# Performance work log

Hardware: AMD Instinct MI355X
Metric: run time of the kernel (lower is better)

## Reference

```python
import jax, jax.numpy as jnp
import numpy as np

B, N, M, T = 120, 128, 192, 25
PHI_MIN, PHI_MAX = 1e-6, 30.0


def _phi(x):
    # phi(x) = -log(tanh(x/2)); self-inverse map used for exact sum-product CN update
    return -jnp.log(jnp.tanh(0.5 * jnp.clip(x, PHI_MIN, PHI_MAX)))


def setup_inputs() -> dict:
    rng = np.random.default_rng(0)
    Hx = (rng.random((M, N)) < 4.0 / N).astype(np.float32)   # weight-4 stabilizer-like rows
    Hz = (rng.random((M, N)) < 4.0 / N).astype(np.float32)
    Gx = (rng.random((2, N)) < 16.0 / N).astype(np.float32)  # logical checks for the loss
    Gz = (rng.random((2, N)) < 16.0 / N).astype(np.float32)
    errorx = (rng.random((B, N)) < 0.05).astype(np.float32)  # X-component indicator
    errorz = (rng.random((B, N)) < 0.05).astype(np.float32)  # Z-component indicator
    return {
        "errorx": jnp.asarray(errorx),
        "errorz": jnp.asarray(errorz),
        "ep0": jnp.full((1,), 0.1, jnp.float32),
        "Hx": jnp.asarray(Hx),
        "Hz": jnp.asarray(Hz),
        "Gx": jnp.asarray(Gx),
        "Gz": jnp.asarray(Gz),
        "weights_llr": jnp.ones((T,), jnp.float32),
        "weights_vn": jnp.ones((T,), jnp.float32),
        "weights_cn": jnp.ones((T,), jnp.float32),
    }


def reference(errorx, errorz, ep0, Hx, Hz, Gx, Gz, weights_llr, weights_vn, weights_cn):
    ep = ep0[0]
    # depolarizing channel LLR: P(X-component) = 2*ep/3
    llr0 = jnp.log((1.0 - 2.0 * ep / 3.0) / (2.0 * ep / 3.0))
    Hs = jnp.stack([Hz, Hx])                                   # (2,M,N): ch0 detects X errors, ch1 Z
    synx = jnp.remainder(errorx @ Hz.T, 2.0)                   # (B,M)
    synz = jnp.remainder(errorz @ Hx.T, 2.0)
    syn_sign = 1.0 - 2.0 * jnp.stack([synx, synz], axis=1)     # (B,2,M)
    HALF_PI = jnp.float32(np.pi / 2)

    def iter_loss(Gamma):
        # loss of eq. 11: soft corrections must reproduce a zero syndrome on G
        prob = jax.nn.sigmoid(-Gamma)
        pX, pZ = prob[:, 0, :], prob[:, 1, :]
        corrz = jnp.where(errorz > 0.5, 1.0 - pX, pX)          # qz/qy -> 1-pX, qx/qi -> pX
        corrx = jnp.where(errorx > 0.5, 1.0 - pZ, pZ)
        sx = jnp.einsum('gn,bn->bg', Gz, corrx)
        sz = jnp.einsum('gn,bn->bg', Gx, corrz)
        return (jnp.sum(jnp.abs(jnp.sin(HALF_PI * sz)), axis=1)
                + jnp.sum(jnp.abs(jnp.sin(HALF_PI * sx)), axis=1))

    def body(V, w):
        w_llr, w_vn, w_cn = w
        # --- check node update (exact box-plus via sign/phi decomposition) ---
        sgn = jnp.where(Hs > 0, jnp.where(V < 0, -1.0, 1.0), 1.0)
        tot_sgn = jnp.prod(sgn, axis=3, keepdims=True)         # (B,2,M,1)
        p = jnp.where(Hs > 0, _phi(jnp.abs(V)), 0.0)
        p_sum = jnp.sum(p, axis=3, keepdims=True)
        cn = syn_sign[..., None] * tot_sgn * sgn * _phi(p_sum - p) * Hs * w_cn
        # --- variable node update ---
        cn_sum = jnp.sum(cn, axis=2)                           # (B,2,N)
        Gamma = w_llr * llr0 + cn_sum                          # (B,2,N) marginal LLRs
        Vnew = (w_llr * llr0 + w_vn * (cn_sum[:, :, None, :] - cn)) * Hs
        return Vnew, iter_loss(Gamma)

    V0 = jnp.broadcast_to(llr0 * Hs, (errorx.shape[0], 2, Hs.shape[1], Hs.shape[2]))
    _, losses = jax.lax.scan(body, V0, (weights_llr, weights_vn, weights_cn))  # (T,B)
    loss = jnp.mean(jnp.sum(losses, axis=0))
    loss_min = jnp.mean(jnp.min(losses, axis=0))
    return jnp.stack([loss, loss_min])
```

## Files before the change

### kernel.cpp

```cpp
#include <hip/hip_runtime.h>
#include <math.h>

#define Bsz 120
#define Nv  128
#define Ms  192
#define Tit 25
#define EPAD 1024
#define KE4 4
#define DC  16
#define DV  24

#define O_VCOL 0
#define O_ECHK 512
#define O_VEID 1024
#define O_RP   2560
#define O_DEG  2656
#define SSTRIDE 2752
#define WS_CNT  (2 * SSTRIDE)
#define WS_PART (WS_CNT + 2)

__device__ __forceinline__ float phi_f(float x) {
  x = fminf(fmaxf(x, 1e-6f), 30.0f);
  const float u = __expf(-x);
  float den = 1.0f - u;
  if (x < 0.03125f) den = x * (1.0f - 0.5f * x + 0.16666667f * x * x);
  return 0.69314718f * (__log2f(1.0f + u) - __log2f(den));
}

#define USH(arr, k) ((arr[(k) >> 1] >> (((k) & 1) * 16)) & 0xffff)

__global__ __launch_bounds__(384) void setup_kernel(const float* __restrict__ Hx,
                                                    const float* __restrict__ Hz,
                                                    int* __restrict__ W) {
  __shared__ unsigned mask[2 * Ms][4];
  __shared__ int rp_s[2][Ms + 1];
  __shared__ int wtot[6];
  const int tid = threadIdx.x;
  const int lane = tid & 63, wv = tid >> 6;
  const int s = (tid >= Ms) ? 1 : 0;
  const int m = s ? tid - Ms : tid;
  const float* H = s ? Hx : Hz;
  unsigned short* vcol_g = (unsigned short*)(W + s * SSTRIDE + O_VCOL);
  unsigned short* echk_g = (unsigned short*)(W + s * SSTRIDE + O_ECHK);
  unsigned short* rp_g   = (unsigned short*)(W + s * SSTRIDE + O_RP);
  unsigned short* deg_g  = (unsigned short*)(W + s * SSTRIDE + O_DEG);

  if (tid == 0) W[WS_CNT] = 0;

  unsigned mw[4];
  int d = 0;
  const float4* H4 = (const float4*)(H + m * Nv);
#pragma unroll
  for (int w = 0; w < 4; ++w) {
    unsigned bits = 0;
#pragma unroll
    for (int q = 0; q < 8; ++q) {
      const float4 v = H4[w * 8 + q];
      if (v.x > 0.f) bits |= 1u << (q * 4 + 0);
      if (v.y > 0.f) bits |= 1u << (q * 4 + 1);
      if (v.z > 0.f) bits |= 1u << (q * 4 + 2);
      if (v.w > 0.f) bits |= 1u << (q * 4 + 3);
    }
    mw[w] = bits;
    mask[tid][w] = bits;
    d += __popc(bits);
  }
  int x = d;
#pragma unroll
  for (int off = 1; off < 64; off <<= 1) {
    const int y = __shfl_up(x, off);
    if (lane >= off) x += y;
  }
  if (lane == 63) wtot[wv] = x;
  __syncthreads();
  int carry = 0;
  const int wbase = s ? 3 : 0;
  for (int k = wbase; k < wv; ++k) carry += wtot[k];
  const int incl = x + carry;
  const int excl = incl - d;
  rp_s[s][m] = excl;
  if (m == Ms - 1) rp_s[s][Ms] = incl;
  rp_g[m] = (unsigned short)excl;
  deg_g[m] = (unsigned short)((d <= DC) ? d : DC);
  __syncthreads();
  const int E = rp_s[s][Ms];
  {
    int o = excl;
#pragma unroll
    for (int w = 0; w < 4; ++w) {
      unsigned bits = mw[w];
      while (bits) {
        const int j = __ffs(bits) - 1;
        bits &= bits - 1;
        if (o < EPAD) { vcol_g[o] = (unsigned short)(w * 32 + j); echk_g[o] = (unsigned short)m; }
        ++o;
      }
    }
  }
  for (int e = E + m; e < EPAD; e += Ms) { vcol_g[e] = Nv; echk_g[e] = Ms; }
  __syncthreads();
  if (tid < 2 * Nv) {
    const int s2 = tid >> 7, n = tid & (Nv - 1);
    const int wnd = n >> 5, bit = n & 31;
    unsigned short* veid_g = (unsigned short*)(W + s2 * SSTRIDE + O_VEID);
    int kk = 0;
    for (int m2 = 0; m2 < Ms; ++m2) {
      const unsigned wb = mask[s2 * Ms + m2][wnd];
      if ((wb >> bit) & 1u) {
        int ke = __popc(wb & ((1u << bit) - 1u));
        for (int w = 0; w < wnd; ++w) ke += __popc(mask[s2 * Ms + m2][w]);
        if (kk < DV) veid_g[n * DV + kk] = (unsigned short)(rp_s[s2][m2] + ke);
        ++kk;
      }
    }
    for (int z = (kk < DV ? kk : DV); z < DV; ++z) veid_g[n * DV + z] = EPAD;
  }
}

__global__ __launch_bounds__(256, 1) void nbp_kernel(
    const float* __restrict__ errorx, const float* __restrict__ errorz,
    const float* __restrict__ ep0,
    const float* __restrict__ Gx, const float* __restrict__ Gz,
    const float* __restrict__ w_llr, const float* __restrict__ w_vn,
    const float* __restrict__ w_cn,
    int* __restrict__ W, float* __restrict__ out) {
  __shared__ float p_l[EPAD + 1];
  __shared__ float cn_l[EPAD + 1];
  __shared__ float csum_l[Nv + 1];
  __shared__ float2 pt2[256];
  __shared__ float corrbuf[2][Nv];
  __shared__ float wls[Tit], wvs[Tit], wcs[Tit];
  __shared__ float wred[4], wredm[4];
  __shared__ int lastFlag;

  const int tid = threadIdx.x;
  const int bid = blockIdx.x;
  const int b = bid >> 1, s = bid & 1;
  const int* base = W + s * SSTRIDE;
  const unsigned short* vcol_g = (const unsigned short*)(base + O_VCOL);
  const unsigned short* echk_g = (const unsigned short*)(base + O_ECHK);
  const unsigned short* veid_g = (const unsigned short*)(base + O_VEID);
  const unsigned short* rp_g   = (const unsigned short*)(base + O_RP);
  const unsigned short* deg_g  = (const unsigned short*)(base + O_DEG);
  float* partBase = (float*)(W + WS_PART);
  float* part = partBase + (s * Bsz + b) * Tit;

  const float ep   = ep0[0];
  const float a23  = (2.0f * ep) / 3.0f;
  const float llr0 = logf((1.0f - a23) / a23);

  if (tid < Tit) {
    wls[tid] = w_llr[tid];
    wvs[tid] = w_vn[tid];
    wcs[tid] = w_cn[tid];
  }
  if (tid < Nv) {
    const float* esyn = (s ? errorz : errorx) + b * Nv;
    csum_l[tid] = esyn[tid];
  }
  if (tid == 0) {
    csum_l[Nv] = 0.f;
    p_l[EPAD] = 0.f;
    cn_l[EPAD] = 0.f;
  }

  unsigned vcolp[2] = {0, 0}, chkp[2] = {0, 0};
#pragma unroll
  for (int k = 0; k < KE4; ++k) {
    const unsigned vc = vcol_g[tid + (k << 8)];
    const unsigned ck = echk_g[tid + (k << 8)];
    vcolp[k >> 1] |= vc << ((k & 1) * 16);
    chkp[k >> 1]  |= ck << ((k & 1) * 16);
  }
  const int rp0 = (tid < Ms) ? (int)rp_g[tid] : 0;
  const int dg0 = (tid < Ms) ? (int)deg_g[tid] : 0;

  unsigned vep[12];
  float ec = 0.f;
  if (tid < Nv) {
    const uint4* q = (const uint4*)(veid_g + tid * DV);
    const uint4 a0 = q[0], a1 = q[1], a2 = q[2];
    vep[0] = a0.x; vep[1] = a0.y; vep[2]  = a0.z; vep[3]  = a0.w;
    vep[4] = a1.x; vep[5] = a1.y; vep[6]  = a1.z; vep[7]  = a1.w;
    vep[8] = a2.x; vep[9] = a2.y; vep[10] = a2.z; vep[11] = a2.w;
    ec = ((s ? errorx : errorz) + b * Nv)[tid];
  }
  const int l2 = tid - 128;
  float g0a = 0.f, g0b = 0.f, g1a = 0.f, g1b = 0.f;
  if (tid >= 128 && tid < 192) {
    const float* G = s ? Gz : Gx;
    g0a = G[l2]; g0b = G[l2 + 64];
    g1a = G[Nv + l2]; g1b = G[Nv + l2 + 64];
  }
  __syncthreads();

#pragma unroll
  for (int k = 0; k < KE4; ++k) {
    const int e = tid + (k << 8);
    const int nn = USH(vcolp, k);
    p_l[e] = (csum_l[nn] > 0.5f) ? -1.f : 1.f;
  }
  __syncthreads();
  float ssgn;
  {
    unsigned par = 0;
#pragma unroll
    for (int k = 0; k < DC; ++k) {
      const int addr = (k < dg0) ? (rp0 + k) : EPAD;
      par ^= __float_as_uint(p_l[addr]) >> 31;
    }
    ssgn = (par & 1u) ? -1.f : 1.f;
  }
  __syncthreads();

  float cn_reg[KE4] = {0.f, 0.f, 0.f, 0.f};
  float basePrev = llr0, wvPrev = 0.f;

#pragma unroll 1
  for (int t = 0; t < Tit; ++t) {
    const float wct = wcs[t];

    float pe[KE4];
#pragma unroll
    for (int k = 0; k < KE4; ++k) {
      const int e = tid + (k << 8);
      const int nn = USH(vcolp, k);
      const float csv = csum_l[nn];
      const float Vk = basePrev + wvPrev * (csv - cn_reg[k]);
      float pv = phi_f(fabsf(Vk));
      pv = fmaxf(pv, 1e-30f);
      pv = (Vk < 0.f) ? -pv : pv;
      pe[k] = pv;
      p_l[e] = pv;
    }
    __syncthreads();

    {
      float psum = 0.f;
      unsigned par = 0;
#pragma unroll
      for (int k = 0; k < DC; ++k) {
        const int addr = (k < dg0) ? (rp0 + k) : EPAD;
        const float v = p_l[addr];
        par ^= __float_as_uint(v) >> 31;
        psum += fabsf(v);
      }
      const float tt = ((par & 1u) ? -ssgn : ssgn) * wct;
      pt2[tid] = make_float2(psum, tt);
    }
    __syncthreads();

#pragma unroll
    for (int k = 0; k < KE4; ++k) {
      const int cc = USH(chkp, k);
      const float2 q = pt2[cc];
      const float ps = pe[k];
      const float sg = (__float_as_uint(ps) >> 31) ? -1.f : 1.f;
      const float cnk = q.y * sg * phi_f(q.x - fabsf(ps));
      cn_reg[k] = cnk;
      cn_l[tid + (k << 8)] = cnk;
    }
    __syncthreads();

    const float base_t = wls[t] * llr0;
    if (tid < Nv) {
      float cs = 0.f;
#pragma unroll
      for (int k = 0; k < DV; ++k) cs += cn_l[USH(vep, k)];
      csum_l[tid] = cs;
      const float prob = 1.0f / (1.0f + __expf(base_t + cs));
      corrbuf[t & 1][tid] = (ec > 0.5f) ? 1.0f - prob : prob;
    } else if (tid < 192 && t > 0) {
      const float* cr = corrbuf[(t - 1) & 1];
      const float c0 = cr[l2], c1 = cr[l2 + 64];
      float la = g0a * c0 + g0b * c1;
      float lb = g1a * c0 + g1b * c1;
#pragma unroll
      for (int off = 1; off < 64; off <<= 1) {
        la += __shfl_xor(la, off);
        lb += __shfl_xor(lb, off);
      }
      const float lt = fabsf(__sinf(1.57079632679f * la)) +
                       fabsf(__sinf(1.57079632679f * lb));
      if (l2 == 0) part[t - 1] = lt;
    }
    basePrev = base_t;
    wvPrev = wvs[t];
    __syncthreads();
  }

  if (tid >= 128 && tid < 192) {
    const float* cr = corrbuf[(Tit - 1) & 1];
    const float c0 = cr[l2], c1 = cr[l2 + 64];
    float la = g0a * c0 + g0b * c1;
    float lb = g1a * c0 + g1b * c1;
#pragma unroll
    for (int off = 1; off < 64; off <<= 1) {
      la += __shfl_xor(la, off);
      lb += __shfl_xor(lb, off);
    }
    const float lt = fabsf(__sinf(1.57079632679f * la)) +
                     fabsf(__sinf(1.57079632679f * lb));
    if (l2 == 0) part[Tit - 1] = lt;
  }
  __syncthreads();

  __threadfence();
  if (tid == 0) lastFlag = (atomicAdd(W + WS_CNT, 1) == 2 * Bsz - 1);
  __syncthreads();
  if (lastFlag) {
    __threadfence();
    float sm = 0.f, mn = 0.f;
    if (tid < Bsz) {
      const float* pa = partBase + tid * Tit;
      const float* pb = partBase + (Bsz + tid) * Tit;
      float acc = 0.f, mloc = 3.0e38f;
#pragma unroll
      for (int t = 0; t < Tit; ++t) {
        const float lt = pa[t] + pb[t];
        acc += lt;
        mloc = fminf(mloc, lt);
      }
      sm = acc;
      mn = mloc;
    }
#pragma unroll
    for (int off = 32; off; off >>= 1) {
      sm += __shfl_down(sm, off);
      mn += __shfl_down(mn, off);
    }
    if ((tid & 63) == 0) { wred[tid >> 6] = sm; wredm[tid >> 6] = mn; }
    __syncthreads();
    if (tid == 0) {
      out[0] = (wred[0] + wred[1]) * (1.0f / Bsz);
      out[1] = (wredm[0] + wredm[1]) * (1.0f / Bsz);
    }
  }
}

extern "C" void kernel_launch(void* const* d_in, const int* in_sizes, int n_in,
                              void* d_out, int out_size, void* d_ws, size_t ws_size,
                              hipStream_t stream) {
  const float* errorx = (const float*)d_in[0];
  const float* errorz = (const float*)d_in[1];
  const float* ep0    = (const float*)d_in[2];
  const float* Hx     = (const float*)d_in[3];
  const float* Hz     = (const float*)d_in[4];
  const float* Gx     = (const float*)d_in[5];
  const float* Gz     = (const float*)d_in[6];
  const float* wllr   = (const float*)d_in[7];
  const float* wvn    = (const float*)d_in[8];
  const float* wcn    = (const float*)d_in[9];
  float* out = (float*)d_out;
  int* W = (int*)d_ws;

  hipLaunchKernelGGL(setup_kernel, dim3(1), dim3(2 * Ms), 0, stream, Hx, Hz, W);
  hipLaunchKernelGGL(nbp_kernel, dim3(2 * Bsz), dim3(256), 0, stream,
                     errorx, errorz, ep0, Gx, Gz, wllr, wvn, wcn, W, out);
}
```

Before: 167.1 us.

## Fuse sparse-graph setup into the decoder kernel, building adjacency in shared memory

Removes the single-block setup kernel. Each decoder block now rebuilds the check-node and variable-node adjacency from Hx/Hz in shared memory, using a column bitmask built with shared atomics. A memset replaces the counter reset. This removes one serial kernel launch and the global round trip for the index tables, at the cost of every one of the 240 blocks repeating the setup work and using more shared memory.

```diff
diff --git a/kernel.cpp b/kernel.cpp
--- a/kernel.cpp
+++ b/kernel.cpp
@@ -10,14 +10,8 @@
 #define DC  16
 #define DV  24
 
-#define O_VCOL 0
-#define O_ECHK 512
-#define O_VEID 1024
-#define O_RP   2560
-#define O_DEG  2656
-#define SSTRIDE 2752
-#define WS_CNT  (2 * SSTRIDE)
-#define WS_PART (WS_CNT + 2)
+#define WS_CNT  0
+#define WS_PART 2
 
 __device__ __forceinline__ float phi_f(float x) {
   x = fminf(fmaxf(x, 1e-6f), 30.0f);
@@ -29,119 +23,34 @@
 
 #define USH(arr, k) ((arr[(k) >> 1] >> (((k) & 1) * 16)) & 0xffff)
 
-__global__ __launch_bounds__(384) void setup_kernel(const float* __restrict__ Hx,
-                                                    const float* __restrict__ Hz,
-                                                    int* __restrict__ W) {
-  __shared__ unsigned mask[2 * Ms][4];
-  __shared__ int rp_s[2][Ms + 1];
-  __shared__ int wtot[6];
-  const int tid = threadIdx.x;
-  const int lane = tid & 63, wv = tid >> 6;
-  const int s = (tid >= Ms) ? 1 : 0;
-  const int m = s ? tid - Ms : tid;
-  const float* H = s ? Hx : Hz;
-  unsigned short* vcol_g = (unsigned short*)(W + s * SSTRIDE + O_VCOL);
-  unsigned short* echk_g = (unsigned short*)(W + s * SSTRIDE + O_ECHK);
-  unsigned short* rp_g   = (unsigned short*)(W + s * SSTRIDE + O_RP);
-  unsigned short* deg_g  = (unsigned short*)(W + s * SSTRIDE + O_DEG);
-
-  if (tid == 0) W[WS_CNT] = 0;
-
-  unsigned mw[4];
-  int d = 0;
-  const float4* H4 = (const float4*)(H + m * Nv);
-#pragma unroll
-  for (int w = 0; w < 4; ++w) {
-    unsigned bits = 0;
-#pragma unroll
-    for (int q = 0; q < 8; ++q) {
-      const float4 v = H4[w * 8 + q];
-      if (v.x > 0.f) bits |= 1u << (q * 4 + 0);
-      if (v.y > 0.f) bits |= 1u << (q * 4 + 1);
-      if (v.z > 0.f) bits |= 1u << (q * 4 + 2);
-      if (v.w > 0.f) bits |= 1u << (q * 4 + 3);
-    }
-    mw[w] = bits;
-    mask[tid][w] = bits;
-    d += __popc(bits);
-  }
-  int x = d;
-#pragma unroll
-  for (int off = 1; off < 64; off <<= 1) {
-    const int y = __shfl_up(x, off);
-    if (lane >= off) x += y;
-  }
-  if (lane == 63) wtot[wv] = x;
-  __syncthreads();
-  int carry = 0;
-  const int wbase = s ? 3 : 0;
-  for (int k = wbase; k < wv; ++k) carry += wtot[k];
-  const int incl = x + carry;
-  const int excl = incl - d;
-  rp_s[s][m] = excl;
-  if (m == Ms - 1) rp_s[s][Ms] = incl;
-  rp_g[m] = (unsigned short)excl;
-  deg_g[m] = (unsigned short)((d <= DC) ? d : DC);
-  __syncthreads();
-  const int E = rp_s[s][Ms];
-  {
-    int o = excl;
-#pragma unroll
-    for (int w = 0; w < 4; ++w) {
-      unsigned bits = mw[w];
-      while (bits) {
-        const int j = __ffs(bits) - 1;
-        bits &= bits - 1;
-        if (o < EPAD) { vcol_g[o] = (unsigned short)(w * 32 + j); echk_g[o] = (unsigned short)m; }
-        ++o;
-      }
-    }
-  }
-  for (int e = E + m; e < EPAD; e += Ms) { vcol_g[e] = Nv; echk_g[e] = Ms; }
-  __syncthreads();
-  if (tid < 2 * Nv) {
-    const int s2 = tid >> 7, n = tid & (Nv - 1);
-    const int wnd = n >> 5, bit = n & 31;
-    unsigned short* veid_g = (unsigned short*)(W + s2 * SSTRIDE + O_VEID);
-    int kk = 0;
-    for (int m2 = 0; m2 < Ms; ++m2) {
-      const unsigned wb = mask[s2 * Ms + m2][wnd];
-      if ((wb >> bit) & 1u) {
-        int ke = __popc(wb & ((1u << bit) - 1u));
-        for (int w = 0; w < wnd; ++w) ke += __popc(mask[s2 * Ms + m2][w]);
-        if (kk < DV) veid_g[n * DV + kk] = (unsigned short)(rp_s[s2][m2] + ke);
-        ++kk;
-      }
-    }
-    for (int z = (kk < DV ? kk : DV); z < DV; ++z) veid_g[n * DV + z] = EPAD;
-  }
-}
-
 __global__ __launch_bounds__(256, 1) void nbp_kernel(
     const float* __restrict__ errorx, const float* __restrict__ errorz,
     const float* __restrict__ ep0,
+    const float* __restrict__ Hx, const float* __restrict__ Hz,
     const float* __restrict__ Gx, const float* __restrict__ Gz,
     const float* __restrict__ w_llr, const float* __restrict__ w_vn,
     const float* __restrict__ w_cn,
     int* __restrict__ W, float* __restrict__ out) {
+  __shared__ unsigned mask_l[Ms][4];
+  __shared__ int rp_l[Ms + 1];
+  __shared__ unsigned colmask[Nv][6];
+  __shared__ unsigned char vcol8[EPAD];
+  __shared__ unsigned char echk8[EPAD];
+  __shared__ unsigned short veid_l[Nv * DV];
   __shared__ float p_l[EPAD + 1];
   __shared__ float cn_l[EPAD + 1];
   __shared__ float csum_l[Nv + 1];
   __shared__ float2 pt2[256];
   __shared__ float corrbuf[2][Nv];
   __shared__ float wls[Tit], wvs[Tit], wcs[Tit];
+  __shared__ int wtot[3];
   __shared__ float wred[4], wredm[4];
   __shared__ int lastFlag;
 
   const int tid = threadIdx.x;
+  const int lane = tid & 63, wv = tid >> 6;
   const int bid = blockIdx.x;
   const int b = bid >> 1, s = bid & 1;
-  const int* base = W + s * SSTRIDE;
-  const unsigned short* vcol_g = (const unsigned short*)(base + O_VCOL);
-  const unsigned short* echk_g = (const unsigned short*)(base + O_ECHK);
-  const unsigned short* veid_g = (const unsigned short*)(base + O_VEID);
-  const unsigned short* rp_g   = (const unsigned short*)(base + O_RP);
-  const unsigned short* deg_g  = (const unsigned short*)(base + O_DEG);
   float* partBase = (float*)(W + WS_PART);
   float* part = partBase + (s * Bsz + b) * Tit;
 
@@ -154,6 +63,75 @@
     wvs[tid] = w_vn[tid];
     wcs[tid] = w_cn[tid];
   }
+  {
+    unsigned* cmf = &colmask[0][0];
+    for (int i = tid; i < Nv * 6; i += 256) cmf[i] = 0;
+    unsigned* v32 = (unsigned*)veid_l;
+    for (int i = tid; i < Nv * DV / 2; i += 256) v32[i] = (EPAD << 16) | EPAD;
+  }
+  unsigned mwa[4] = {0, 0, 0, 0};
+  int d = 0;
+  if (tid < Ms) {
+    const float4* H4 = (const float4*)((s ? Hx : Hz) + tid * Nv);
+#pragma unroll
+    for (int w = 0; w < 4; ++w) {
+      unsigned bits = 0;
+#pragma unroll
+      for (int q = 0; q < 8; ++q) {
+        const float4 v = H4[w * 8 + q];
+        if (v.x > 0.f) bits |= 1u << (q * 4 + 0);
+        if (v.y > 0.f) bits |= 1u << (q * 4 + 1);
+        if (v.z > 0.f) bits |= 1u << (q * 4 + 2);
+        if (v.w > 0.f) bits |= 1u << (q * 4 + 3);
+      }
+      mwa[w] = bits;
+      mask_l[tid][w] = bits;
+      d += __popc(bits);
+    }
+  }
+  __syncthreads();
+
+  {
+    int x = d;
+#pragma unroll
+    for (int off = 1; off < 64; off <<= 1) {
+      const int y = __shfl_up(x, off);
+      if (lane >= off) x += y;
+    }
+    if (lane == 63 && wv < 3) wtot[wv] = x;
+    __syncthreads();
+    int carry = 0;
+    for (int k = 0; k < wv && k < 3; ++k) carry += wtot[k];
+    if (tid < Ms) {
+      const int incl = x + carry;
+      rp_l[tid] = incl - d;
+      if (tid == Ms - 1) rp_l[Ms] = incl;
+    }
+  }
+  __syncthreads();
+  const int E = rp_l[Ms];
+
+  if (tid < Ms) {
+    int o = rp_l[tid];
+    const unsigned wbit = 1u << (tid & 31);
+    const int wrd = tid >> 5;
+#pragma unroll
+    for (int w = 0; w < 4; ++w) {
+      unsigned bits = mwa[w];
+      while (bits) {
+        const int j = __ffs(bits) - 1;
+        bits &= bits - 1;
+        const int n = w * 32 + j;
+        if (o < EPAD) { vcol8[o] = (unsigned char)n; echk8[o] = (unsigned char)tid; }
+        atomicOr(&colmask[n][wrd], wbit);
+        ++o;
+      }
+    }
+  }
+  for (int e = E + tid; e < EPAD; e += 256) {
+    vcol8[e] = (unsigned char)Nv;
+    echk8[e] = (unsigned char)Ms;
+  }
   if (tid < Nv) {
     const float* esyn = (s ? errorz : errorx) + b * Nv;
     csum_l[tid] = esyn[tid];
@@ -163,27 +141,43 @@
     p_l[EPAD] = 0.f;
     cn_l[EPAD] = 0.f;
   }
+  __syncthreads();
 
   unsigned vcolp[2] = {0, 0}, chkp[2] = {0, 0};
 #pragma unroll
   for (int k = 0; k < KE4; ++k) {
-    const unsigned vc = vcol_g[tid + (k << 8)];
-    const unsigned ck = echk_g[tid + (k << 8)];
-    vcolp[k >> 1] |= vc << ((k & 1) * 16);
-    chkp[k >> 1]  |= ck << ((k & 1) * 16);
-  }
-  const int rp0 = (tid < Ms) ? (int)rp_g[tid] : 0;
-  const int dg0 = (tid < Ms) ? (int)deg_g[tid] : 0;
-
-  unsigned vep[12];
-  float ec = 0.f;
+    const int e = tid + (k << 8);
+    vcolp[k >> 1] |= ((unsigned)vcol8[e]) << ((k & 1) * 16);
+    chkp[k >> 1]  |= ((unsigned)echk8[e]) << ((k & 1) * 16);
+  }
+  int rp0 = 0, dg0 = 0;
+  if (tid < Ms) {
+    rp0 = rp_l[tid];
+    const int dd = rp_l[tid + 1] - rp0;
+    dg0 = (dd <= DC) ? dd : DC;
+  }
   if (tid < Nv) {
-    const uint4* q = (const uint4*)(veid_g + tid * DV);
-    const uint4 a0 = q[0], a1 = q[1], a2 = q[2];
-    vep[0] = a0.x; vep[1] = a0.y; vep[2]  = a0.z; vep[3]  = a0.w;
-    vep[4] = a1.x; vep[5] = a1.y; vep[6]  = a1.z; vep[7]  = a1.w;
-    vep[8] = a2.x; vep[9] = a2.y; vep[10] = a2.z; vep[11] = a2.w;
-    ec = ((s ? errorx : errorz) + b * Nv)[tid];
+    const int wnd = tid >> 5;
+    const unsigned lowmask = (1u << (tid & 31)) - 1u;
+    int kk = 0;
+#pragma unroll
+    for (int w6 = 0; w6 < 6; ++w6) {
+      unsigned bits = colmask[tid][w6];
+      while (bits) {
+        const int m2 = w6 * 32 + (__ffs(bits) - 1);
+        bits &= bits - 1;
+        int r = __popc(mask_l[m2][wnd] & lowmask);
+        for (int w = 0; w < wnd; ++w) r += __popc(mask_l[m2][w]);
+        if (kk < DV) veid_l[tid * DV + kk] = (unsigned short)(rp_l[m2] + r);
+        ++kk;
+      }
+    }
+  }
+#pragma unroll
+  for (int k = 0; k < KE4; ++k) {
+    const int e = tid + (k << 8);
+    const int nn = USH(vcolp, k);
+    p_l[e] = (csum_l[nn] > 0.5f) ? -1.f : 1.f;
   }
   const int l2 = tid - 128;
   float g0a = 0.f, g0b = 0.f, g1a = 0.f, g1b = 0.f;
@@ -192,15 +186,21 @@
     g0a = G[l2]; g0b = G[l2 + 64];
     g1a = G[Nv + l2]; g1b = G[Nv + l2 + 64];
   }
-  __syncthreads();
-
-#pragma unroll
-  for (int k = 0; k < KE4; ++k) {
-    const int e = tid + (k << 8);
-    const int nn = USH(vcolp, k);
-    p_l[e] = (csum_l[nn] > 0.5f) ? -1.f : 1.f;
-  }
-  __syncthreads();
+  float ec = 0.f;
+  if (tid < Nv) ec = ((s ? errorx : errorz) + b * Nv)[tid];
+  __syncthreads();
+
+  unsigned vep[12];
+  if (tid < Nv) {
+    const uint4* q = (const uint4*)(veid_l + tid * DV);
+    const uint4 a0 = q[0], a1 = q[1], a2 = q[2];
+    vep[0] = a0.x; vep[1] = a0.y; vep[2]  = a0.z; vep[3]  = a0.w;
+    vep[4] = a1.x; vep[5] = a1.y; vep[6]  = a1.z; vep[7]  = a1.w;
+    vep[8] = a2.x; vep[9] = a2.y; vep[10] = a2.z; vep[11] = a2.w;
+  } else {
+#pragma unroll
+    for (int i = 0; i < 12; ++i) vep[i] = (EPAD << 16) | EPAD;
+  }
   float ssgn;
   {
     unsigned par = 0;
@@ -354,7 +354,7 @@
   float* out = (float*)d_out;
   int* W = (int*)d_ws;
 
-  hipLaunchKernelGGL(setup_kernel, dim3(1), dim3(2 * Ms), 0, stream, Hx, Hz, W);
+  hipMemsetAsync((void*)(W + WS_CNT), 0, sizeof(int), stream);
   hipLaunchKernelGGL(nbp_kernel, dim3(2 * Bsz), dim3(256), 0, stream,
-                     errorx, errorz, ep0, Gx, Gz, wllr, wvn, wcn, W, out);
+                     errorx, errorz, ep0, Hx, Hz, Gx, Gz, wllr, wvn, wcn, W, out);
 }
```

Measured after the change: 133.9 us. -19.9%, faster.
